# Optimization experiments

Measured on AMD Instinct MI355X. Metric: run time of the kernel, lower is better.

## Reference

```python
import math
import jax, jax.numpy as jnp
import numpy as np

B, T, D, H = 4, 2048, 1024, 16
HD = D // H


def setup_inputs() -> dict:
    key = jax.random.key(0)
    ks = jax.random.split(key, 5)
    s = 1.0 / math.sqrt(D)  # linear-layer-ish init scale
    x = jax.random.normal(ks[0], (B, T, D), dtype=jnp.float32)
    wq = jax.random.normal(ks[1], (D, D), dtype=jnp.float32) * s
    wk = jax.random.normal(ks[2], (D, D), dtype=jnp.float32) * s
    wv = jax.random.normal(ks[3], (D, D), dtype=jnp.float32) * s
    wo = jax.random.normal(ks[4], (D, D), dtype=jnp.float32) * s
    bq = jnp.zeros((D,), jnp.float32)
    bk = jnp.zeros((D,), jnp.float32)
    bv = jnp.zeros((D,), jnp.float32)
    bo = jnp.zeros((D,), jnp.float32)
    # causal 0/1 mask, broadcast over batch and heads: [1, 1, T, T]
    mask = jnp.tril(jnp.ones((T, T), jnp.int32))[None, None]
    return {"x": x, "wq": wq, "bq": bq, "wk": wk, "bk": bk,
            "wv": wv, "bv": bv, "wo": wo, "bo": bo, "mask": mask}


def reference(x, wq, bq, wk, bk, wv, bv, wo, bo, mask):
    b, t, d = x.shape
    # separate QKV linears (x_cond defaults to x -> self-attention)
    q = x @ wq.T + bq
    k = x @ wk.T + bk
    v = x @ wv.T + bv
    # [b, t, h, hd] -> [b, h, t, hd]
    q = q.reshape(b, t, H, HD).transpose(0, 2, 1, 3)
    k = k.reshape(b, t, H, HD).transpose(0, 2, 1, 3)
    v = v.reshape(b, t, H, HD).transpose(0, 2, 1, 3)
    scale = 1.0 / math.sqrt(HD)
    attn = jnp.einsum('bhtd,bhsd->bhts', q, k) * scale  # [b, h, t, t]
    attn = jnp.where(mask[:, :, :t, :t] == 0, jnp.float32(-jnp.inf), attn)
    attn = jax.nn.softmax(attn, axis=-1)
    # dropout is identity in eval mode
    out = jnp.einsum('bhts,bhsd->bhtd', attn, v)  # [b, h, t, hd]
    out = out.transpose(0, 2, 1, 3).reshape(b, t, d)
    return out @ wo.T + bo
```

## Files before the change

### kernel.cpp

```cpp
#include <hip/hip_runtime.h>
#include <cstdint>

typedef __bf16 bf16x8 __attribute__((ext_vector_type(8)));
typedef float f32x4 __attribute__((ext_vector_type(4)));
typedef uint32_t u32x4 __attribute__((ext_vector_type(4)));
typedef unsigned short u16;

#define B_ 4
#define T_ 2048
#define D_ 1024
#define H_ 16
#define HD_ 64
#define M_ (B_*T_)
#define QSCALE 0.1803368801111204f

__device__ __forceinline__ u16 f2bf(float f) {
  union { float f; uint32_t u; } x; x.f = f;
  uint32_t u = x.u;
  uint32_t r = (u + 0x7FFFu + ((u >> 16) & 1u)) >> 16;
  return (u16)r;
}

__device__ __forceinline__ uint32_t pkbf(float a, float b) {
  union { float f; uint32_t u; } x, y; x.f = a; y.f = b;
  uint32_t t0 = x.u + 0x8000u, t1 = y.u + 0x8000u;
  return __builtin_amdgcn_perm(t1, t0, 0x07060302u);
}

__device__ __forceinline__ bf16x8 ld8(const u16* p) {
  return *(const bf16x8*)p;
}

__device__ __forceinline__ void gl_lds16(const u16* g, u16* l) {
  __builtin_amdgcn_global_load_lds(
      (__attribute__((address_space(1))) void*)(g),
      (__attribute__((address_space(3))) void*)(l), 16, 0, 0);
}

__global__ void cvt_all(const float* __restrict__ x, const float* __restrict__ wq,
                        const float* __restrict__ wk, const float* __restrict__ wv,
                        const float* __restrict__ wo,
                        u16* __restrict__ xb, u16* __restrict__ wqb, u16* __restrict__ wkb,
                        u16* __restrict__ wvb, u16* __restrict__ wob) {
  const long NX = (long)M_ * D_;
  long i = ((long)blockIdx.x * 256 + threadIdx.x) * 4;
  const float* s; u16* d; long j;
  if (i < NX) { s = x; d = xb; j = i; }
  else {
    long r = i - NX; int seg = (int)(r >> 20); j = r & ((1 << 20) - 1);
    s = seg == 0 ? wq : seg == 1 ? wk : seg == 2 ? wv : wo;
    d = seg == 0 ? wqb : seg == 1 ? wkb : seg == 2 ? wvb : wob;
  }
  float4 v = *(const float4*)(s + j);
  ushort4 o;
  o.x = f2bf(v.x); o.y = f2bf(v.y); o.z = f2bf(v.z); o.w = f2bf(v.w);
  *(ushort4*)(d + j) = o;
}


template <int PH>
__device__ __forceinline__ void ldA_ph(bf16x8 (&af)[2][2], const u16* buf,
                                       int wr, int lanem, int quad) {
#pragma unroll
  for (int mi = 0; mi < 2; ++mi)
#pragma unroll
    for (int ks = 0; ks < 2; ++ks) {
      int row = wr * 64 + (PH * 2 + mi) * 16 + lanem;
      int off = row * 64 + ((ks * 32 + quad * 8) ^ ((lanem & 7) << 3));
      af[mi][ks] = ld8(buf + off);
    }
}

__device__ __forceinline__ void ldB_all(bf16x8 (&bfr)[4][2], const u16* buf,
                                        int wc, int lanem, int quad) {
#pragma unroll
  for (int nj = 0; nj < 4; ++nj)
#pragma unroll
    for (int ks = 0; ks < 2; ++ks) {
      int row = 256 + wc * 64 + nj * 16 + lanem;
      int off = row * 64 + ((ks * 32 + quad * 8) ^ ((lanem & 7) << 3));
      bfr[nj][ks] = ld8(buf + off);
    }
}

template <int PH>
__device__ __forceinline__ void mfmaPH(f32x4 (&acc)[4][4], const bf16x8 (&af)[2][2],
                                       const bf16x8 (&bfr)[4][2]) {
#pragma unroll
  for (int mi = 0; mi < 2; ++mi)
#pragma unroll
    for (int nj = 0; nj < 4; ++nj)
#pragma unroll
      for (int ks = 0; ks < 2; ++ks)
        acc[PH * 2 + mi][nj] = __builtin_amdgcn_mfma_f32_16x16x32_bf16(
            af[mi][ks], bfr[nj][ks], acc[PH * 2 + mi][nj], 0, 0, 0);
}

#define PH_PRE()                                        \
  __builtin_amdgcn_s_barrier();                         \
  asm volatile("s_waitcnt lgkmcnt(0)" ::: "memory");    \
  __builtin_amdgcn_sched_barrier(0);                    \
  __builtin_amdgcn_s_setprio(1)

#define PH_POST()                                       \
  __builtin_amdgcn_s_setprio(0);                        \
  __builtin_amdgcn_s_barrier()

__global__ __launch_bounds__(512, 2)
void gemm_qkv(const u16* __restrict__ A, const u16* __restrict__ Bw,
              const float* __restrict__ bq, const float* __restrict__ bk,
              const float* __restrict__ bv,
              u16* __restrict__ qb, u16* __restrict__ kb, u16* __restrict__ vtb) {
  __shared__ union {
    u16 S[3][384][64];
    u16 C[256 * 136];
  } sm;

  const int tid = threadIdx.x;
  const int wv = tid >> 6, lane = tid & 63;
  const int lanem = lane & 15, quad = lane >> 4;
  const int wr = wv >> 1, wc = wv & 1;

  const int l = ((int)blockIdx.x & 7) * 96 + ((int)blockIdx.x >> 3);
  const int n0 = (l % 24) * 128, m0 = (l / 24) * 256;

  const int grow = lane >> 3;
  const int gcol = (((lane & 7) ^ grow) * 8);

  auto stage = [&](u16* bufbase, int u, int k0) {
    const u16* src = (u < 4)
        ? A  + (size_t)(m0 + u * 64 + wv * 8 + grow) * D_ + k0 + gcol
        : Bw + (size_t)(n0 + (u - 4) * 64 + wv * 8 + grow) * D_ + k0 + gcol;
    gl_lds16(src, bufbase + (u * 64 + wv * 8) * 64);
  };

  f32x4 acc[4][4];
#pragma unroll
  for (int a = 0; a < 4; ++a)
#pragma unroll
    for (int b = 0; b < 4; ++b) acc[a][b] = (f32x4){0.f, 0.f, 0.f, 0.f};

  bf16x8 af[2][2];
  bf16x8 bfr[4][2];

  u16* p0 = &sm.S[0][0][0];
  u16* p1 = &sm.S[1][0][0];
  u16* p2 = &sm.S[2][0][0];

#pragma unroll
  for (int u = 0; u < 6; ++u) stage(p0, u, 0);
#pragma unroll
  for (int u = 0; u < 6; ++u) stage(p1, u, 64);
  asm volatile("s_waitcnt vmcnt(6)" ::: "memory");
  __builtin_amdgcn_s_barrier();

  for (int kt = 0; kt < 16; ++kt) {
    const int k2 = (kt + 2) << 6;

    ldA_ph<0>(af, p0, wr, lanem, quad);
    ldB_all(bfr, p0, wc, lanem, quad);
    if (kt < 14) { stage(p2, 0, k2); stage(p2, 1, k2); stage(p2, 2, k2); }
    PH_PRE();
    mfmaPH<0>(acc, af, bfr);
    PH_POST();

    ldA_ph<1>(af, p0, wr, lanem, quad);
    if (kt < 14) { stage(p2, 3, k2); stage(p2, 4, k2); stage(p2, 5, k2); }
    __builtin_amdgcn_s_barrier();
    asm volatile("s_waitcnt lgkmcnt(0)" ::: "memory");
    __builtin_amdgcn_sched_barrier(0);
    __builtin_amdgcn_s_setprio(1);
    mfmaPH<1>(acc, af, bfr);
    __builtin_amdgcn_s_setprio(0);
    if (kt < 14)       asm volatile("s_waitcnt vmcnt(6)" ::: "memory");
    else if (kt == 14) asm volatile("s_waitcnt vmcnt(0)" ::: "memory");
    __builtin_amdgcn_s_barrier();

    u16* t = p0; p0 = p1; p1 = p2; p2 = t;
  }

  const int seg = n0 >> 10, n0l = n0 & 1023;
  const int bb = m0 >> 11, tl0 = m0 & (T_ - 1);

  if (seg == 2) {
    __syncthreads();
#pragma unroll
    for (int a = 0; a < 4; ++a)
#pragma unroll
      for (int nj = 0; nj < 4; ++nj) {
        int ncol = wc * 64 + nj * 16 + lanem;
        float bvv = bv[n0l + ncol];
        int mb = wr * 64 + a * 16 + quad * 4;
        ushort4 w4;
        w4.x = f2bf(acc[a][nj][0] + bvv);
        w4.y = f2bf(acc[a][nj][1] + bvv);
        w4.z = f2bf(acc[a][nj][2] + bvv);
        w4.w = f2bf(acc[a][nj][3] + bvv);
        *(ushort4*)&sm.C[ncol * 264 + mb] = w4;
      }
    __syncthreads();
#pragma unroll
    for (int it = 0; it < 8; ++it) {
      int chunk = it * 512 + tid;
      int nrow = chunk >> 5, c8 = chunk & 31;
      int gnl = n0l + nrow;
      int hh = gnl >> 6, hd = gnl & 63;
      *(uint4*)&vtb[(((size_t)bb * H_ + hh) * HD_ + hd) * T_ + tl0 + c8 * 8] =
          *(const uint4*)&sm.C[nrow * 264 + c8 * 8];
    }
  } else {
    const float* bias = seg == 0 ? bq : bk;
    u16* out = seg == 0 ? qb : kb;
    const float sc = seg == 0 ? QSCALE : 1.0f;
    __syncthreads();
#pragma unroll
    for (int a = 0; a < 4; ++a)
#pragma unroll
      for (int nj = 0; nj < 4; ++nj) {
        int col = wc * 64 + nj * 16 + lanem;
        float bvv = bias[n0l + col];
        int r = wr * 64 + a * 16 + quad * 4;
#pragma unroll
        for (int i = 0; i < 4; ++i)
          sm.C[(r + i) * 136 + col] = f2bf((acc[a][nj][i] + bvv) * sc);
      }
    __syncthreads();
#pragma unroll
    for (int it = 0; it < 8; ++it) {
      int chunk = it * 512 + tid;
      int row = chunk >> 4, c8 = chunk & 15;
      int col0 = c8 * 8;
      int hh = (n0l + col0) >> 6, hd = col0 & 63;
      int t = tl0 + row;
      *(uint4*)&out[(((size_t)bb * H_ + hh) * T_ + t) * HD_ + hd] =
          *(const uint4*)&sm.C[row * 136 + col0];
    }
  }
}

__global__ __launch_bounds__(256, 3)
void gemm_wo(const u16* __restrict__ A, const u16* __restrict__ Bw,
             const float* __restrict__ bias, float* __restrict__ Co) {
  __shared__ u16 S[2][2][4096];
  int tid = threadIdx.x;
  int n0 = blockIdx.x * 128, m0 = blockIdx.y * 128;
  int wv = tid >> 6, lane = tid & 63, lanem = lane & 15, quad = lane >> 4;
  int wm = (wv >> 1) * 64, wn = (wv & 1) * 64;

  int rA = wv * 16 + (lane >> 2);
  int cc = (lane & 3) * 8;
  const u16* Ab = A + (size_t)(m0 + rA) * D_ + cc;
  const u16* Bb = Bw + (size_t)(n0 + rA) * D_ + cc;

  f32x4 acc[4][4];
#pragma unroll
  for (int mi = 0; mi < 4; ++mi)
#pragma unroll
    for (int ni = 0; ni < 4; ++ni)
      acc[mi][ni] = (f32x4){0.f, 0.f, 0.f, 0.f};

  for (int kt = 0; kt < 16; ++kt) {
    int k0 = kt * 64;
    __syncthreads();
#pragma unroll
    for (int ks = 0; ks < 2; ++ks)
#pragma unroll
      for (int j = 0; j < 2; ++j) {
        gl_lds16(Ab + k0 + ks * 32 + (size_t)j * 64 * D_,
                 &S[0][ks][(j * 256 + wv * 64) * 8]);
        gl_lds16(Bb + k0 + ks * 32 + (size_t)j * 64 * D_,
                 &S[1][ks][(j * 256 + wv * 64) * 8]);
      }
    __syncthreads();
#pragma unroll
    for (int ks = 0; ks < 2; ++ks) {
      bf16x8 af[4], bfr[4];
#pragma unroll
      for (int mi = 0; mi < 4; ++mi)
        af[mi] = ld8(&S[0][ks][(wm + mi * 16 + lanem) * 32 + quad * 8]);
#pragma unroll
      for (int ni = 0; ni < 4; ++ni)
        bfr[ni] = ld8(&S[1][ks][(wn + ni * 16 + lanem) * 32 + quad * 8]);
#pragma unroll
      for (int mi = 0; mi < 4; ++mi)
#pragma unroll
        for (int ni = 0; ni < 4; ++ni)
          acc[mi][ni] = __builtin_amdgcn_mfma_f32_16x16x32_bf16(af[mi], bfr[ni], acc[mi][ni], 0, 0, 0);
    }
  }

#pragma unroll
  for (int ni = 0; ni < 4; ++ni) {
    int gn = n0 + wn + ni * 16 + lanem;
    float bvv = bias[gn];
#pragma unroll
    for (int mi = 0; mi < 4; ++mi)
#pragma unroll
      for (int i = 0; i < 4; ++i) {
        int gm = m0 + wm + mi * 16 + quad * 4 + i;
        Co[(size_t)gm * D_ + gn] = acc[mi][ni][i] + bvv;
      }
  }
}

__global__ __launch_bounds__(256, 4)
void flash4(const u16* __restrict__ qb, const u16* __restrict__ kb,
            const u16* __restrict__ vtb, u16* __restrict__ ob) {
  __shared__ u16 Ks[2][2][64][32];
  __shared__ u16 Vs[2][2][64][32];
  int tid = threadIdx.x, wv = tid >> 6, lane = tid & 63;
  int lanem = lane & 15, quad = lane >> 4;
  int h = blockIdx.y, b = blockIdx.z;
  int z = (int)blockIdx.z;
  int qt = ((int)blockIdx.x ^ ((z & 1) * 15) ^ ((z >> 1) * 3)) & 15;
  size_t bh = (size_t)b * H_ + h;
  int qrow0 = qt * 128 + wv * 32;
  const u16* Qg = qb + (bh * T_ + qrow0) * HD_;
  const u16* Kg = kb + bh * T_ * HD_;
  const u16* Vg = vtb + bh * HD_ * T_;

  int slot = tid >> 2, r = slot & 15;
  int key = (slot >> 5) * 32 + (r >> 2) * 8 + ((slot >> 4) & 1) * 4 + (r & 3);
  const u16* gK = Kg + (size_t)key * HD_ + (tid & 3) * 8;
  const u16* gV = Vg + (size_t)slot * T_ + (tid & 3) * 8;

  bf16x8 bq[2][2];
#pragma unroll
  for (int mi = 0; mi < 2; ++mi)
#pragma unroll
    for (int ks = 0; ks < 2; ++ks)
      bq[mi][ks] = ld8(&Qg[(size_t)(mi * 16 + lanem) * HD_ + ks * 32 + quad * 8]);

  f32x4 acc_o[2][4];
  float lsum[2][4];
#pragma unroll
  for (int mi = 0; mi < 2; ++mi) {
#pragma unroll
    for (int c = 0; c < 4; ++c) lsum[mi][c] = 0.f;
#pragma unroll
    for (int ni = 0; ni < 4; ++ni) acc_o[mi][ni] = (f32x4){0.f, 0.f, 0.f, 0.f};
  }

  int nIter = qt * 2 + 2;
  int myTiles = (qrow0 >> 6) + 1;

#define STAGE_KV(bufi, s0c)                                                 \
  do {                                                                      \
    gl_lds16(gK + (size_t)(s0c) * HD_,      &Ks[bufi][0][0][0] + wv * 512); \
    gl_lds16(gK + (size_t)(s0c) * HD_ + 32, &Ks[bufi][1][0][0] + wv * 512); \
    gl_lds16(gV + (s0c),                    &Vs[bufi][0][0][0] + wv * 512); \
    gl_lds16(gV + (s0c) + 32,               &Vs[bufi][1][0][0] + wv * 512); \
  } while (0)

  STAGE_KV(0, 0);
  for (int it = 0; it < nIter; ++it) {
    __builtin_amdgcn_s_waitcnt(0);
    __syncthreads();
    if (it + 1 < nIter) STAGE_KV((it + 1) & 1, (it + 1) * 64);
    if (it >= myTiles) continue;
    int s0 = it * 64, buf = it & 1;

    f32x4 accs[2][4];
#pragma unroll
    for (int mi = 0; mi < 2; ++mi)
#pragma unroll
      for (int ni = 0; ni < 4; ++ni) accs[mi][ni] = (f32x4){0.f, 0.f, 0.f, 0.f};
#pragma unroll
    for (int ks = 0; ks < 2; ++ks)
#pragma unroll
      for (int ni = 0; ni < 4; ++ni) {
        bf16x8 kf = ld8(&Ks[buf][ks][ni * 16 + lanem][quad * 8]);
        accs[0][ni] = __builtin_amdgcn_mfma_f32_16x16x32_bf16(kf, bq[0][ks], accs[0][ni], 0, 0, 0);
        accs[1][ni] = __builtin_amdgcn_mfma_f32_16x16x32_bf16(kf, bq[1][ks], accs[1][ni], 0, 0, 0);
      }

    if (s0 + 63 > qrow0) {
#pragma unroll
      for (int mi = 0; mi < 2; ++mi) {
        int qg = qrow0 + mi * 16 + lanem;
#pragma unroll
        for (int ni = 0; ni < 4; ++ni)
#pragma unroll
          for (int i = 0; i < 4; ++i) {
            int sl = (ni >> 1) * 32 + quad * 8 + (ni & 1) * 4 + i;
            float p = (s0 + sl > qg) ? 0.f : __builtin_amdgcn_exp2f(accs[mi][ni][i]);
            accs[mi][ni][i] = p;
            lsum[mi][i] += p;
          }
      }
    } else {
#pragma unroll
      for (int mi = 0; mi < 2; ++mi)
#pragma unroll
        for (int ni = 0; ni < 4; ++ni)
#pragma unroll
          for (int i = 0; i < 4; ++i) {
            float p = __builtin_amdgcn_exp2f(accs[mi][ni][i]);
            accs[mi][ni][i] = p;
            lsum[mi][i] += p;
          }
    }

#pragma unroll
    for (int c = 0; c < 2; ++c) {
      u32x4 pk0, pk1;
      pk0[0] = pkbf(accs[0][c * 2][0], accs[0][c * 2][1]);
      pk0[1] = pkbf(accs[0][c * 2][2], accs[0][c * 2][3]);
      pk0[2] = pkbf(accs[0][c * 2 + 1][0], accs[0][c * 2 + 1][1]);
      pk0[3] = pkbf(accs[0][c * 2 + 1][2], accs[0][c * 2 + 1][3]);
      pk1[0] = pkbf(accs[1][c * 2][0], accs[1][c * 2][1]);
      pk1[1] = pkbf(accs[1][c * 2][2], accs[1][c * 2][3]);
      pk1[2] = pkbf(accs[1][c * 2 + 1][0], accs[1][c * 2 + 1][1]);
      pk1[3] = pkbf(accs[1][c * 2 + 1][2], accs[1][c * 2 + 1][3]);
      bf16x8 bp0 = __builtin_bit_cast(bf16x8, pk0);
      bf16x8 bp1 = __builtin_bit_cast(bf16x8, pk1);
#pragma unroll
      for (int ni = 0; ni < 4; ++ni) {
        bf16x8 vf = ld8(&Vs[buf][c][ni * 16 + lanem][quad * 8]);
        acc_o[0][ni] = __builtin_amdgcn_mfma_f32_16x16x32_bf16(vf, bp0, acc_o[0][ni], 0, 0, 0);
        acc_o[1][ni] = __builtin_amdgcn_mfma_f32_16x16x32_bf16(vf, bp1, acc_o[1][ni], 0, 0, 0);
      }
    }
  }
#undef STAGE_KV

#pragma unroll
  for (int mi = 0; mi < 2; ++mi) {
    float v = (lsum[mi][0] + lsum[mi][1]) + (lsum[mi][2] + lsum[mi][3]);
    v += __shfl_xor(v, 16);
    v += __shfl_xor(v, 32);
    float inv = 1.f / v;
    int q = qrow0 + mi * 16 + lanem;
    u16* og = ob + ((size_t)b * T_ + q) * D_ + h * HD_;
#pragma unroll
    for (int ni = 0; ni < 4; ++ni) {
      ushort4 st;
      st.x = f2bf(acc_o[mi][ni][0] * inv);
      st.y = f2bf(acc_o[mi][ni][1] * inv);
      st.z = f2bf(acc_o[mi][ni][2] * inv);
      st.w = f2bf(acc_o[mi][ni][3] * inv);
      *(ushort4*)(og + ni * 16 + quad * 4) = st;
    }
  }
}

extern "C" void kernel_launch(void* const* d_in, const int* in_sizes, int n_in,
                              void* d_out, int out_size, void* d_ws, size_t ws_size,
                              hipStream_t stream) {
  const float* x  = (const float*)d_in[0];
  const float* wq = (const float*)d_in[1];
  const float* bq = (const float*)d_in[2];
  const float* wk = (const float*)d_in[3];
  const float* bk = (const float*)d_in[4];
  const float* wv = (const float*)d_in[5];
  const float* bv = (const float*)d_in[6];
  const float* wo = (const float*)d_in[7];
  const float* bo = (const float*)d_in[8];

  char* ws = (char*)d_ws;
  const size_t MB = 1ull << 20;
  u16* xb   = (u16*)(ws + 0 * MB);
  u16* wqkv = (u16*)(ws + 16 * MB);
  u16* wob  = (u16*)(ws + 22 * MB);
  u16* qb   = (u16*)(ws + 24 * MB);
  u16* kb   = (u16*)(ws + 40 * MB);
  u16* vtb  = (u16*)(ws + 56 * MB);
  u16* ob   = (u16*)(ws + 72 * MB);

  cvt_all<<<(M_ * D_ + 4 * D_ * D_) / 1024, 256, 0, stream>>>(
      x, wq, wk, wv, wo, xb, wqkv, wqkv + (size_t)D_ * D_, wqkv + 2 * (size_t)D_ * D_, wob);

  gemm_qkv<<<768, 512, 0, stream>>>(xb, wqkv, bq, bk, bv, qb, kb, vtb);

  flash4<<<dim3(T_ / 128, H_, B_), 256, 0, stream>>>(qb, kb, vtb, ob);

  gemm_wo<<<dim3(D_ / 128, M_ / 128), 256, 0, stream>>>(ob, wob, bo, (float*)d_out);
}
```

Measured before the change: 269.5 us.

## Software-pipeline LDS fragment loads in QKV GEMM and swizzle flash K/V tiles

The QKV GEMM main loop now double-buffers register fragments. The next tile's A/B fragments load from LDS while the current phase's MFMAs run, using partial lgkmcnt waits in place of full drains. Separately, the flash attention kernel stores K and V tiles as 64x64 rows with an XOR swizzle on the 16-byte column chunk, aiming to cut LDS bank conflicts on fragment reads. These changes raise register pressure and depend on hand-tuned waitcnt values whose correctness is delicate.

```diff
diff --git a/kernel.cpp b/kernel.cpp
--- a/kernel.cpp
+++ b/kernel.cpp
@@ -96,15 +96,10 @@
             af[mi][ks], bfr[nj][ks], acc[PH * 2 + mi][nj], 0, 0, 0);
 }
 
-#define PH_PRE()                                        \
+#define SBAR()                                          \
+  __builtin_amdgcn_sched_barrier(0);                    \
   __builtin_amdgcn_s_barrier();                         \
-  asm volatile("s_waitcnt lgkmcnt(0)" ::: "memory");    \
-  __builtin_amdgcn_sched_barrier(0);                    \
-  __builtin_amdgcn_s_setprio(1)
-
-#define PH_POST()                                       \
-  __builtin_amdgcn_s_setprio(0);                        \
-  __builtin_amdgcn_s_barrier()
+  __builtin_amdgcn_sched_barrier(0)
 
 __global__ __launch_bounds__(512, 2)
 void gemm_qkv(const u16* __restrict__ A, const u16* __restrict__ Bw,
@@ -140,8 +135,8 @@
 #pragma unroll
     for (int b = 0; b < 4; ++b) acc[a][b] = (f32x4){0.f, 0.f, 0.f, 0.f};
 
-  bf16x8 af[2][2];
-  bf16x8 bfr[4][2];
+  bf16x8 afA[2][2], afB[2][2];
+  bf16x8 bf2[2][4][2];
 
   u16* p0 = &sm.S[0][0][0];
   u16* p1 = &sm.S[1][0][0];
@@ -153,28 +148,39 @@
   for (int u = 0; u < 6; ++u) stage(p1, u, 64);
   asm volatile("s_waitcnt vmcnt(6)" ::: "memory");
   __builtin_amdgcn_s_barrier();
-
+  __builtin_amdgcn_sched_barrier(0);
+  ldA_ph<0>(afA, p0, wr, lanem, quad);
+  ldB_all(bf2[0], p0, wc, lanem, quad);
+
+#pragma unroll 2
   for (int kt = 0; kt < 16; ++kt) {
     const int k2 = (kt + 2) << 6;
 
-    ldA_ph<0>(af, p0, wr, lanem, quad);
-    ldB_all(bfr, p0, wc, lanem, quad);
+    ldA_ph<1>(afB, p0, wr, lanem, quad);
     if (kt < 14) { stage(p2, 0, k2); stage(p2, 1, k2); stage(p2, 2, k2); }
-    PH_PRE();
-    mfmaPH<0>(acc, af, bfr);
-    PH_POST();
-
-    ldA_ph<1>(af, p0, wr, lanem, quad);
-    if (kt < 14) { stage(p2, 3, k2); stage(p2, 4, k2); stage(p2, 5, k2); }
-    __builtin_amdgcn_s_barrier();
-    asm volatile("s_waitcnt lgkmcnt(0)" ::: "memory");
+    SBAR();
+    asm volatile("s_waitcnt lgkmcnt(4)" ::: "memory");
     __builtin_amdgcn_sched_barrier(0);
     __builtin_amdgcn_s_setprio(1);
-    mfmaPH<1>(acc, af, bfr);
+    mfmaPH<0>(acc, afA, bf2[kt & 1]);
     __builtin_amdgcn_s_setprio(0);
-    if (kt < 14)       asm volatile("s_waitcnt vmcnt(6)" ::: "memory");
+    if (kt < 14)       asm volatile("s_waitcnt vmcnt(3)" ::: "memory");
     else if (kt == 14) asm volatile("s_waitcnt vmcnt(0)" ::: "memory");
-    __builtin_amdgcn_s_barrier();
+    SBAR();
+
+    if (kt < 15) {
+      ldA_ph<0>(afA, p1, wr, lanem, quad);
+      ldB_all(bf2[(kt + 1) & 1], p1, wc, lanem, quad);
+    }
+    if (kt < 14) { stage(p2, 3, k2); stage(p2, 4, k2); stage(p2, 5, k2); }
+    SBAR();
+    if (kt < 15) asm volatile("s_waitcnt lgkmcnt(12)" ::: "memory");
+    else         asm volatile("s_waitcnt lgkmcnt(0)" ::: "memory");
+    __builtin_amdgcn_sched_barrier(0);
+    __builtin_amdgcn_s_setprio(1);
+    mfmaPH<1>(acc, afB, bf2[kt & 1]);
+    __builtin_amdgcn_s_setprio(0);
+    SBAR();
 
     u16* t = p0; p0 = p1; p1 = p2; p2 = t;
   }
@@ -306,8 +312,8 @@
 __global__ __launch_bounds__(256, 4)
 void flash4(const u16* __restrict__ qb, const u16* __restrict__ kb,
             const u16* __restrict__ vtb, u16* __restrict__ ob) {
-  __shared__ u16 Ks[2][2][64][32];
-  __shared__ u16 Vs[2][2][64][32];
+  __shared__ u16 Ks[2][64][64];
+  __shared__ u16 Vs[2][64][64];
   int tid = threadIdx.x, wv = tid >> 6, lane = tid & 63;
   int lanem = lane & 15, quad = lane >> 4;
   int h = blockIdx.y, b = blockIdx.z;
@@ -319,10 +325,16 @@
   const u16* Kg = kb + bh * T_ * HD_;
   const u16* Vg = vtb + bh * HD_ * T_;
 
-  int slot = tid >> 2, r = slot & 15;
-  int key = (slot >> 5) * 32 + (r >> 2) * 8 + ((slot >> 4) & 1) * 4 + (r & 3);
-  const u16* gK = Kg + (size_t)key * HD_ + (tid & 3) * 8;
-  const u16* gV = Vg + (size_t)slot * T_ + (tid & 3) * 8;
+  int r8 = lane >> 3, c8 = lane & 7;
+  int scol = ((c8 ^ r8) * 8);
+  int slot0 = wv * 8 + r8, slot1 = 32 + wv * 8 + r8;
+  auto keyf = [](int s) {
+    return (s >> 5) * 32 + (((s & 15) >> 2) * 8) + (((s >> 4) & 1) * 4) + (s & 3);
+  };
+  const u16* gK0 = Kg + (size_t)keyf(slot0) * HD_ + scol;
+  const u16* gK1 = Kg + (size_t)keyf(slot1) * HD_ + scol;
+  const u16* gV0 = Vg + (size_t)slot0 * T_ + scol;
+  const u16* gV1 = Vg + (size_t)slot1 * T_ + scol;
 
   bf16x8 bq[2][2];
 #pragma unroll
@@ -344,12 +356,12 @@
   int nIter = qt * 2 + 2;
   int myTiles = (qrow0 >> 6) + 1;
 
-#define STAGE_KV(bufi, s0c)                                                 \
-  do {                                                                      \
-    gl_lds16(gK + (size_t)(s0c) * HD_,      &Ks[bufi][0][0][0] + wv * 512); \
-    gl_lds16(gK + (size_t)(s0c) * HD_ + 32, &Ks[bufi][1][0][0] + wv * 512); \
-    gl_lds16(gV + (s0c),                    &Vs[bufi][0][0][0] + wv * 512); \
-    gl_lds16(gV + (s0c) + 32,               &Vs[bufi][1][0][0] + wv * 512); \
+#define STAGE_KV(bufi, s0c)                                              \
+  do {                                                                   \
+    gl_lds16(gK0 + (size_t)(s0c) * HD_, &Ks[bufi][0][0] + slot0 * 64 - r8 * 64); \
+    gl_lds16(gK1 + (size_t)(s0c) * HD_, &Ks[bufi][0][0] + slot1 * 64 - r8 * 64); \
+    gl_lds16(gV0 + (s0c),               &Vs[bufi][0][0] + slot0 * 64 - r8 * 64); \
+    gl_lds16(gV1 + (s0c),               &Vs[bufi][0][0] + slot1 * 64 - r8 * 64); \
   } while (0)
 
   STAGE_KV(0, 0);
@@ -359,6 +371,8 @@
     if (it + 1 < nIter) STAGE_KV((it + 1) & 1, (it + 1) * 64);
     if (it >= myTiles) continue;
     int s0 = it * 64, buf = it & 1;
+    const u16* Kb = &Ks[buf][0][0];
+    const u16* Vb = &Vs[buf][0][0];
 
     f32x4 accs[2][4];
 #pragma unroll
@@ -369,7 +383,8 @@
     for (int ks = 0; ks < 2; ++ks)
 #pragma unroll
       for (int ni = 0; ni < 4; ++ni) {
-        bf16x8 kf = ld8(&Ks[buf][ks][ni * 16 + lanem][quad * 8]);
+        int row = ni * 16 + lanem;
+        bf16x8 kf = ld8(Kb + row * 64 + (((ks * 4 + quad) ^ (lanem & 7)) * 8));
         accs[0][ni] = __builtin_amdgcn_mfma_f32_16x16x32_bf16(kf, bq[0][ks], accs[0][ni], 0, 0, 0);
         accs[1][ni] = __builtin_amdgcn_mfma_f32_16x16x32_bf16(kf, bq[1][ks], accs[1][ni], 0, 0, 0);
       }
@@ -416,7 +431,8 @@
       bf16x8 bp1 = __builtin_bit_cast(bf16x8, pk1);
 #pragma unroll
       for (int ni = 0; ni < 4; ++ni) {
-        bf16x8 vf = ld8(&Vs[buf][c][ni * 16 + lanem][quad * 8]);
+        int row = ni * 16 + lanem;
+        bf16x8 vf = ld8(Vb + row * 64 + (((c * 4 + quad) ^ (lanem & 7)) * 8));
         acc_o[0][ni] = __builtin_amdgcn_mfma_f32_16x16x32_bf16(vf, bp0, acc_o[0][ni], 0, 0, 0);
         acc_o[1][ni] = __builtin_amdgcn_mfma_f32_16x16x32_bf16(vf, bp1, acc_o[1][ni], 0, 0, 0);
       }
```

New measurement: 266.2 us. No clear change (-1.2%).

## Reuse triple-buffered pipelined QKV GEMM mainloop for output projection GEMM

Applied to the files above, without the earlier changes.

Factors the QKV GEMM's triple-buffered, swizzled, priority-scheduled k-loop into a macro and uses it for the output projection GEMM as well. The Wo GEMM moves from 128x128 tiles with 256 threads and a single-buffered, sync-heavy loop to 256x128 tiles with 512 threads, prefetching two stages ahead, plus a remapped block order for L2 locality. The aim is to overlap global loads with MFMA work and cut barrier stalls. The catch is that the grid shrinks to 256 blocks, which may underfill the GPU's CUs.

```diff
diff --git a/kernel.cpp b/kernel.cpp
--- a/kernel.cpp
+++ b/kernel.cpp
@@ -106,6 +106,44 @@
   __builtin_amdgcn_s_setprio(0);                        \
   __builtin_amdgcn_s_barrier()
 
+#define GEMM_V3_KLOOP(Asrc, Bsrc)                                              \
+  u16* p0 = &sm.S[0][0][0];                                                    \
+  u16* p1 = &sm.S[1][0][0];                                                    \
+  u16* p2 = &sm.S[2][0][0];                                                    \
+  auto stage = [&](u16* bufbase, int u, int k0) {                              \
+    const u16* src = (u < 4)                                                   \
+        ? Asrc + (size_t)(m0 + u * 64 + wv * 8 + grow) * D_ + k0 + gcol        \
+        : Bsrc + (size_t)(n0 + (u - 4) * 64 + wv * 8 + grow) * D_ + k0 + gcol; \
+    gl_lds16(src, bufbase + (u * 64 + wv * 8) * 64);                           \
+  };                                                                           \
+  _Pragma("unroll")                                                            \
+  for (int u = 0; u < 6; ++u) stage(p0, u, 0);                                 \
+  _Pragma("unroll")                                                            \
+  for (int u = 0; u < 6; ++u) stage(p1, u, 64);                                \
+  asm volatile("s_waitcnt vmcnt(6)" ::: "memory");                             \
+  __builtin_amdgcn_s_barrier();                                                \
+  for (int kt = 0; kt < 16; ++kt) {                                            \
+    const int k2 = (kt + 2) << 6;                                              \
+    ldA_ph<0>(af, p0, wr, lanem, quad);                                        \
+    ldB_all(bfr, p0, wc, lanem, quad);                                         \
+    if (kt < 14) { stage(p2, 0, k2); stage(p2, 1, k2); stage(p2, 2, k2); }     \
+    PH_PRE();                                                                  \
+    mfmaPH<0>(acc, af, bfr);                                                   \
+    PH_POST();                                                                 \
+    ldA_ph<1>(af, p0, wr, lanem, quad);                                        \
+    if (kt < 14) { stage(p2, 3, k2); stage(p2, 4, k2); stage(p2, 5, k2); }     \
+    __builtin_amdgcn_s_barrier();                                              \
+    asm volatile("s_waitcnt lgkmcnt(0)" ::: "memory");                         \
+    __builtin_amdgcn_sched_barrier(0);                                         \
+    __builtin_amdgcn_s_setprio(1);                                             \
+    mfmaPH<1>(acc, af, bfr);                                                   \
+    __builtin_amdgcn_s_setprio(0);                                             \
+    if (kt < 14)       asm volatile("s_waitcnt vmcnt(6)" ::: "memory");        \
+    else if (kt == 14) asm volatile("s_waitcnt vmcnt(0)" ::: "memory");        \
+    __builtin_amdgcn_s_barrier();                                              \
+    u16* t = p0; p0 = p1; p1 = p2; p2 = t;                                     \
+  }
+
 __global__ __launch_bounds__(512, 2)
 void gemm_qkv(const u16* __restrict__ A, const u16* __restrict__ Bw,
               const float* __restrict__ bq, const float* __restrict__ bk,
@@ -127,13 +165,6 @@
   const int grow = lane >> 3;
   const int gcol = (((lane & 7) ^ grow) * 8);
 
-  auto stage = [&](u16* bufbase, int u, int k0) {
-    const u16* src = (u < 4)
-        ? A  + (size_t)(m0 + u * 64 + wv * 8 + grow) * D_ + k0 + gcol
-        : Bw + (size_t)(n0 + (u - 4) * 64 + wv * 8 + grow) * D_ + k0 + gcol;
-    gl_lds16(src, bufbase + (u * 64 + wv * 8) * 64);
-  };
-
   f32x4 acc[4][4];
 #pragma unroll
   for (int a = 0; a < 4; ++a)
@@ -143,41 +174,7 @@
   bf16x8 af[2][2];
   bf16x8 bfr[4][2];
 
-  u16* p0 = &sm.S[0][0][0];
-  u16* p1 = &sm.S[1][0][0];
-  u16* p2 = &sm.S[2][0][0];
-
-#pragma unroll
-  for (int u = 0; u < 6; ++u) stage(p0, u, 0);
-#pragma unroll
-  for (int u = 0; u < 6; ++u) stage(p1, u, 64);
-  asm volatile("s_waitcnt vmcnt(6)" ::: "memory");
-  __builtin_amdgcn_s_barrier();
-
-  for (int kt = 0; kt < 16; ++kt) {
-    const int k2 = (kt + 2) << 6;
-
-    ldA_ph<0>(af, p0, wr, lanem, quad);
-    ldB_all(bfr, p0, wc, lanem, quad);
-    if (kt < 14) { stage(p2, 0, k2); stage(p2, 1, k2); stage(p2, 2, k2); }
-    PH_PRE();
-    mfmaPH<0>(acc, af, bfr);
-    PH_POST();
-
-    ldA_ph<1>(af, p0, wr, lanem, quad);
-    if (kt < 14) { stage(p2, 3, k2); stage(p2, 4, k2); stage(p2, 5, k2); }
-    __builtin_amdgcn_s_barrier();
-    asm volatile("s_waitcnt lgkmcnt(0)" ::: "memory");
-    __builtin_amdgcn_sched_barrier(0);
-    __builtin_amdgcn_s_setprio(1);
-    mfmaPH<1>(acc, af, bfr);
-    __builtin_amdgcn_s_setprio(0);
-    if (kt < 14)       asm volatile("s_waitcnt vmcnt(6)" ::: "memory");
-    else if (kt == 14) asm volatile("s_waitcnt vmcnt(0)" ::: "memory");
-    __builtin_amdgcn_s_barrier();
-
-    u16* t = p0; p0 = p1; p1 = p2; p2 = t;
-  }
+  GEMM_V3_KLOOP(A, Bw);
 
   const int seg = n0 >> 10, n0l = n0 & 1023;
   const int bb = m0 >> 11, tl0 = m0 & (T_ - 1);
@@ -238,67 +235,46 @@
   }
 }
 
-__global__ __launch_bounds__(256, 3)
+__global__ __launch_bounds__(512, 2)
 void gemm_wo(const u16* __restrict__ A, const u16* __restrict__ Bw,
              const float* __restrict__ bias, float* __restrict__ Co) {
-  __shared__ u16 S[2][2][4096];
-  int tid = threadIdx.x;
-  int n0 = blockIdx.x * 128, m0 = blockIdx.y * 128;
-  int wv = tid >> 6, lane = tid & 63, lanem = lane & 15, quad = lane >> 4;
-  int wm = (wv >> 1) * 64, wn = (wv & 1) * 64;
-
-  int rA = wv * 16 + (lane >> 2);
-  int cc = (lane & 3) * 8;
-  const u16* Ab = A + (size_t)(m0 + rA) * D_ + cc;
-  const u16* Bb = Bw + (size_t)(n0 + rA) * D_ + cc;
+  __shared__ union {
+    u16 S[3][384][64];
+    u16 C[256 * 136];
+  } sm;
+
+  const int tid = threadIdx.x;
+  const int wv = tid >> 6, lane = tid & 63;
+  const int lanem = lane & 15, quad = lane >> 4;
+  const int wr = wv >> 1, wc = wv & 1;
+
+  const int l = ((int)blockIdx.x & 7) * 32 + ((int)blockIdx.x >> 3);
+  const int n0 = (l & 7) * 128, m0 = (l >> 3) * 256;
+
+  const int grow = lane >> 3;
+  const int gcol = (((lane & 7) ^ grow) * 8);
 
   f32x4 acc[4][4];
 #pragma unroll
-  for (int mi = 0; mi < 4; ++mi)
-#pragma unroll
-    for (int ni = 0; ni < 4; ++ni)
-      acc[mi][ni] = (f32x4){0.f, 0.f, 0.f, 0.f};
-
-  for (int kt = 0; kt < 16; ++kt) {
-    int k0 = kt * 64;
-    __syncthreads();
-#pragma unroll
-    for (int ks = 0; ks < 2; ++ks)
-#pragma unroll
-      for (int j = 0; j < 2; ++j) {
-        gl_lds16(Ab + k0 + ks * 32 + (size_t)j * 64 * D_,
-                 &S[0][ks][(j * 256 + wv * 64) * 8]);
-        gl_lds16(Bb + k0 + ks * 32 + (size_t)j * 64 * D_,
-                 &S[1][ks][(j * 256 + wv * 64) * 8]);
-      }
-    __syncthreads();
-#pragma unroll
-    for (int ks = 0; ks < 2; ++ks) {
-      bf16x8 af[4], bfr[4];
-#pragma unroll
-      for (int mi = 0; mi < 4; ++mi)
-        af[mi] = ld8(&S[0][ks][(wm + mi * 16 + lanem) * 32 + quad * 8]);
-#pragma unroll
-      for (int ni = 0; ni < 4; ++ni)
-        bfr[ni] = ld8(&S[1][ks][(wn + ni * 16 + lanem) * 32 + quad * 8]);
-#pragma unroll
-      for (int mi = 0; mi < 4; ++mi)
-#pragma unroll
-        for (int ni = 0; ni < 4; ++ni)
-          acc[mi][ni] = __builtin_amdgcn_mfma_f32_16x16x32_bf16(af[mi], bfr[ni], acc[mi][ni], 0, 0, 0);
-    }
-  }
-
-#pragma unroll
-  for (int ni = 0; ni < 4; ++ni) {
-    int gn = n0 + wn + ni * 16 + lanem;
+  for (int a = 0; a < 4; ++a)
+#pragma unroll
+    for (int b = 0; b < 4; ++b) acc[a][b] = (f32x4){0.f, 0.f, 0.f, 0.f};
+
+  bf16x8 af[2][2];
+  bf16x8 bfr[4][2];
+
+  GEMM_V3_KLOOP(A, Bw);
+
+#pragma unroll
+  for (int nj = 0; nj < 4; ++nj) {
+    int gn = n0 + wc * 64 + nj * 16 + lanem;
     float bvv = bias[gn];
 #pragma unroll
-    for (int mi = 0; mi < 4; ++mi)
+    for (int a = 0; a < 4; ++a)
 #pragma unroll
       for (int i = 0; i < 4; ++i) {
-        int gm = m0 + wm + mi * 16 + quad * 4 + i;
-        Co[(size_t)gm * D_ + gn] = acc[mi][ni][i] + bvv;
+        int gm = m0 + wr * 64 + a * 16 + quad * 4 + i;
+        Co[(size_t)gm * D_ + gn] = acc[a][nj][i] + bvv;
       }
   }
 }
@@ -474,5 +450,5 @@
 
   flash4<<<dim3(T_ / 128, H_, B_), 256, 0, stream>>>(qb, kb, vtb, ob);
 
-  gemm_wo<<<dim3(D_ / 128, M_ / 128), 256, 0, stream>>>(ob, wob, bo, (float*)d_out);
-}
+  gemm_wo<<<256, 512, 0, stream>>>(ob, wob, bo, (float*)d_out);
+}
```

Measured after the change: 257.9 us. 4.3% less time.
